# Performance work log

Measured on AMD Instinct MI355X. Metric: run time of the kernel, lower is better.

## Reference

```python
import jax, jax.numpy as jnp
import numpy as np
import itertools

B = 128
K = 3            # number of element types == len(n_list)
C_IN = 256
C_OUT = 256
N_LIST = [3, 3, 3]  # L = 9, P = 9!/(3!3!3!) = 1680


def _build_mask():
    # multiset [0,0,0,1,1,1,2,2,2]; distinct permutations of it
    base = []
    for i, n in enumerate(N_LIST):
        base += [i] * n
    perms = sorted(set(itertools.permutations(base)))  # deterministic order
    idx = np.array(perms, dtype=np.int32)              # (P, L)
    # M[a, p, l] = 1.0 iff idx[p, l] == a  -> (K, P, L) binary mask
    M = np.stack([(idx == a).astype(np.float32) for a in range(K)], 0)
    return jnp.asarray(M), idx.shape[1]


def setup_inputs() -> dict:
    key = jax.random.key(0)
    kx, kw = jax.random.split(key)
    M, L = _build_mask()
    x = jax.random.normal(kx, (B, L, C_IN), dtype=jnp.float32)
    # weightParameter: (k, channels_out, channels_in)
    W = jax.random.normal(kw, (K, C_OUT, C_IN), dtype=jnp.float32)
    return {"x": x, "W": W, "M": M}


def reference(x, W, M):
    # Original: for each type a, W_a = x @ W[a].T (B,L,Cout), then
    # y += einsum('BNC,PN->BPC', W_a, M[a]).  Fused over the k loop:
    # Z[b,l,a,o] = sum_c x[b,l,c] * W[a,o,c]   (small: B*L*K*Cout)
    Z = jnp.einsum('blc,koc->blko', x, W)
    # y[b,p,o] = sum_{a,l} Z[b,l,a,o] * M[a,p,l]
    y = jnp.einsum('blko,kpl->bpo', Z, M)
    return y
```

## Files before the change

kernel.cpp:

```cpp
#include <hip/hip_runtime.h>

#define B_DIM 128
#define L_DIM 9
#define K_DIM 3
#define C 256
#define P_TOT 1680
#define R_DIM 27
#define CHUNK 210

#define WS_WT_OFF 16384
#define WS_Z_OFF  (1u << 20)

typedef float vfloat4 __attribute__((ext_vector_type(4)));

__device__ inline float4 add4(float4 a, float4 b) {
    return make_float4(a.x + b.x, a.y + b.y, a.z + b.z, a.w + b.w);
}

__global__ __launch_bounds__(256) void setup_kernel(const float* __restrict__ M,
                                                    const float* __restrict__ W,
                                                    uint2* __restrict__ packed,
                                                    float* __restrict__ Wt) {
    int bid = blockIdx.x;
    int t = threadIdx.x;
    if (bid < 7) {
        int p = bid * 256 + t;
        if (p >= P_TOT) return;
        unsigned rows[L_DIM];
#pragma unroll
        for (int l = 0; l < L_DIM; ++l) {
            float m1 = M[(1 * P_TOT + p) * L_DIM + l];
            float m2 = M[(2 * P_TOT + p) * L_DIM + l];
            unsigned a = (unsigned)(m1 + 2.0f * m2 + 0.5f);
            rows[l] = (unsigned)(l * K_DIM) + a;
        }
        unsigned d = 0;
        if (p > 0) {
            while (d < L_DIM) {
                float m1 = M[(1 * P_TOT + (p - 1)) * L_DIM + d];
                float m2 = M[(2 * P_TOT + (p - 1)) * L_DIM + d];
                unsigned pr = d * K_DIM + (unsigned)(m1 + 2.0f * m2 + 0.5f);
                if (pr != rows[d]) break;
                ++d;
            }
        }
        unsigned lo = 0, hi = 0;
#pragma unroll
        for (int l = 0; l < 6; ++l) lo |= rows[l] << (5 * l);
#pragma unroll
        for (int l = 6; l < L_DIM; ++l) hi |= rows[l] << (5 * (l - 6));
        hi |= d << 15;
        packed[p] = make_uint2(lo, hi);
    } else {
        int tb = bid - 7;
#pragma unroll
        for (int i = 0; i < 4; ++i) {
            int rowid = tb * 4 + i;
            int a = rowid >> 8;
            int c = rowid & 255;
            Wt[(a * C + c) * C + t] = W[(a * C + t) * C + c];
        }
    }
}

__global__ __launch_bounds__(384) void z_kernel(const float* __restrict__ x,
                                                const float* __restrict__ Wt,
                                                float* __restrict__ Z) {
    int bid = blockIdx.x;
    int b = bid >> 1;
    int t = threadIdx.x;
    int a = t >> 7;
    int o = ((bid & 1) << 7) + (t & 127);

    const float4* __restrict__ xb4 = (const float4*)(x + (size_t)b * (L_DIM * C));
    const float* __restrict__ wp = Wt + (size_t)a * C * C + o;

    float acc[L_DIM];
#pragma unroll
    for (int l = 0; l < L_DIM; ++l) acc[l] = 0.0f;

#pragma unroll 2
    for (int c4 = 0; c4 < C / 4; ++c4) {
        float w0 = wp[(4 * c4 + 0) * C];
        float w1 = wp[(4 * c4 + 1) * C];
        float w2 = wp[(4 * c4 + 2) * C];
        float w3 = wp[(4 * c4 + 3) * C];
#pragma unroll
        for (int l = 0; l < L_DIM; ++l) {
            float4 xv = xb4[l * (C / 4) + c4];
            acc[l] += xv.x * w0 + xv.y * w1 + xv.z * w2 + xv.w * w3;
        }
    }
#pragma unroll
    for (int l = 0; l < L_DIM; ++l)
        Z[((size_t)b * R_DIM + (l * K_DIM + a)) * C + o] = acc[l];
}

__global__ __launch_bounds__(256) void stream_kernel(const float* __restrict__ Z,
                                                     const uint2* __restrict__ packed,
                                                     float* __restrict__ out) {
    __shared__ float Zs[R_DIM * C];
    __shared__ uint2 pk[CHUNK];

    int bid = blockIdx.x;
    int b = bid >> 3;
    int pstart = (bid & 7) * CHUNK;
    int t = threadIdx.x;

    const float4* zg = (const float4*)(Z + (size_t)b * R_DIM * C);
#pragma unroll
    for (int k = 0; k < 7; ++k) {
        int idx = k * 256 + t;
        if (idx < R_DIM * C / 4) ((float4*)Zs)[idx] = zg[idx];
    }
    if (t < CHUNK) pk[t] = packed[pstart + t];
    __syncthreads();

    int wave = t >> 6;
    int lane = t & 63;
    const float4* zsr = (const float4*)Zs;
    vfloat4* out4 = (vfloat4*)out;

    int pb = (CHUNK * wave) >> 2;
    int pe = (CHUNK * (wave + 1)) >> 2;

    float4 p0, p1, p2, p3, p4, p5, p6, p7, p8;

    for (int pl = pb; pl < pe; ++pl) {
        uint2 w = pk[pl];
        unsigned lo = __builtin_amdgcn_readfirstlane(w.x);
        unsigned hi = __builtin_amdgcn_readfirstlane(w.y);
        int k = (pl == pb) ? 0 : (int)(hi >> 15);
        switch (k) {
            case 0: p0 = zsr[(lo & 31u) * 64 + lane]; [[fallthrough]];
            case 1: p1 = add4(p0, zsr[((lo >> 5) & 31u) * 64 + lane]); [[fallthrough]];
            case 2: p2 = add4(p1, zsr[((lo >> 10) & 31u) * 64 + lane]); [[fallthrough]];
            case 3: p3 = add4(p2, zsr[((lo >> 15) & 31u) * 64 + lane]); [[fallthrough]];
            case 4: p4 = add4(p3, zsr[((lo >> 20) & 31u) * 64 + lane]); [[fallthrough]];
            case 5: p5 = add4(p4, zsr[((lo >> 25) & 31u) * 64 + lane]); [[fallthrough]];
            case 6: p6 = add4(p5, zsr[(hi & 31u) * 64 + lane]); [[fallthrough]];
            case 7: p7 = add4(p6, zsr[((hi >> 5) & 31u) * 64 + lane]); [[fallthrough]];
            case 8: p8 = add4(p7, zsr[((hi >> 10) & 31u) * 64 + lane]); break;
            default: break;
        }
        size_t orow = (size_t)(b * P_TOT + pstart + pl);
        vfloat4 sv = {p8.x, p8.y, p8.z, p8.w};
        __builtin_nontemporal_store(sv, &out4[orow * 64 + lane]);
    }
}

extern "C" void kernel_launch(void* const* d_in, const int* in_sizes, int n_in,
                              void* d_out, int out_size, void* d_ws, size_t ws_size,
                              hipStream_t stream) {
    const float* x = (const float*)d_in[0];
    const float* W = (const float*)d_in[1];
    const float* M = (const float*)d_in[2];
    float* out = (float*)d_out;

    uint2* packed = (uint2*)d_ws;
    float* Wt = (float*)((char*)d_ws + WS_WT_OFF);
    float* Z = (float*)((char*)d_ws + WS_Z_OFF);

    setup_kernel<<<199, 256, 0, stream>>>(M, W, packed, Wt);
    z_kernel<<<256, 384, 0, stream>>>(x, Wt, Z);
    stream_kernel<<<1024, 256, 0, stream>>>(Z, packed, out);
}
```

Before: 272.0 us.

## Replace prefix-sum reuse with pairwise-sum lookup table in stream kernel

Instead of reusing prefix sums across consecutive permutations, each block builds a shared-memory table of all pairwise sums for four position pairs (36 rows) plus the last position's three rows. Each output row then takes five table loads and four adds with a single 32-bit packed index, rather than a variable-length chain of up to nine loads with a divergent switch. The stream kernel also moves to 512-thread blocks with 420-row chunks, halving the block count. The cost is the table-building prologue per block and more shared memory. The kernel is output-store bound, so the gain depends on whether the loop was limited by issue or by memory.

```diff
diff --git a/kernel.cpp b/kernel.cpp
--- a/kernel.cpp
+++ b/kernel.cpp
@@ -6,7 +6,8 @@
 #define C 256
 #define P_TOT 1680
 #define R_DIM 27
-#define CHUNK 210
+#define CHUNK 420
+#define LUT_ROWS 39
 
 #define WS_WT_OFF 16384
 #define WS_Z_OFF  (1u << 20)
@@ -19,46 +20,34 @@
 
 __global__ __launch_bounds__(256) void setup_kernel(const float* __restrict__ M,
                                                     const float* __restrict__ W,
-                                                    uint2* __restrict__ packed,
+                                                    unsigned* __restrict__ pkg,
                                                     float* __restrict__ Wt) {
     int bid = blockIdx.x;
     int t = threadIdx.x;
     if (bid < 7) {
         int p = bid * 256 + t;
         if (p >= P_TOT) return;
-        unsigned rows[L_DIM];
+        unsigned a[L_DIM];
 #pragma unroll
         for (int l = 0; l < L_DIM; ++l) {
             float m1 = M[(1 * P_TOT + p) * L_DIM + l];
             float m2 = M[(2 * P_TOT + p) * L_DIM + l];
-            unsigned a = (unsigned)(m1 + 2.0f * m2 + 0.5f);
-            rows[l] = (unsigned)(l * K_DIM) + a;
+            a[l] = (unsigned)(m1 + 2.0f * m2 + 0.5f);
         }
-        unsigned d = 0;
-        if (p > 0) {
-            while (d < L_DIM) {
-                float m1 = M[(1 * P_TOT + (p - 1)) * L_DIM + d];
-                float m2 = M[(2 * P_TOT + (p - 1)) * L_DIM + d];
-                unsigned pr = d * K_DIM + (unsigned)(m1 + 2.0f * m2 + 0.5f);
-                if (pr != rows[d]) break;
-                ++d;
-            }
-        }
-        unsigned lo = 0, hi = 0;
+        unsigned w = 0;
 #pragma unroll
-        for (int l = 0; l < 6; ++l) lo |= rows[l] << (5 * l);
-#pragma unroll
-        for (int l = 6; l < L_DIM; ++l) hi |= rows[l] << (5 * (l - 6));
-        hi |= d << 15;
-        packed[p] = make_uint2(lo, hi);
+        for (int j = 0; j < 4; ++j)
+            w |= (unsigned)(j * 9 + a[2 * j] * 3 + a[2 * j + 1]) << (6 * j);
+        w |= (36u + a[8]) << 24;
+        pkg[p] = w;
     } else {
         int tb = bid - 7;
 #pragma unroll
         for (int i = 0; i < 4; ++i) {
             int rowid = tb * 4 + i;
-            int a = rowid >> 8;
+            int aa = rowid >> 8;
             int c = rowid & 255;
-            Wt[(a * C + c) * C + t] = W[(a * C + t) * C + c];
+            Wt[(aa * C + c) * C + t] = W[(aa * C + t) * C + c];
         }
     }
 }
@@ -96,55 +85,59 @@
         Z[((size_t)b * R_DIM + (l * K_DIM + a)) * C + o] = acc[l];
 }
 
-__global__ __launch_bounds__(256) void stream_kernel(const float* __restrict__ Z,
-                                                     const uint2* __restrict__ packed,
+__global__ __launch_bounds__(512) void stream_kernel(const float* __restrict__ Z,
+                                                     const unsigned* __restrict__ pkg,
                                                      float* __restrict__ out) {
-    __shared__ float Zs[R_DIM * C];
-    __shared__ uint2 pk[CHUNK];
+    __shared__ float lut[LUT_ROWS * C];
+    __shared__ unsigned pk[CHUNK];
 
     int bid = blockIdx.x;
-    int b = bid >> 3;
-    int pstart = (bid & 7) * CHUNK;
+    int b = bid >> 2;
+    int pstart = (bid & 3) * CHUNK;
     int t = threadIdx.x;
 
     const float4* zg = (const float4*)(Z + (size_t)b * R_DIM * C);
+    float4* lutw = (float4*)lut;
 #pragma unroll
-    for (int k = 0; k < 7; ++k) {
-        int idx = k * 256 + t;
-        if (idx < R_DIM * C / 4) ((float4*)Zs)[idx] = zg[idx];
+    for (int it = 0; it < 5; ++it) {
+        int idx = it * 512 + t;
+        if (idx < LUT_ROWS * 64) {
+            int r = idx >> 6, q = idx & 63;
+            float4 v;
+            if (r < 36) {
+                int j = r / 9;
+                int cmb = r - j * 9;
+                int a0 = cmb / 3;
+                int a1 = cmb - a0 * 3;
+                v = add4(zg[(6 * j + a0) * 64 + q], zg[(6 * j + 3 + a1) * 64 + q]);
+            } else {
+                v = zg[(24 + r - 36) * 64 + q];
+            }
+            lutw[idx] = v;
+        }
     }
-    if (t < CHUNK) pk[t] = packed[pstart + t];
+    if (t < CHUNK) pk[t] = pkg[pstart + t];
     __syncthreads();
 
     int wave = t >> 6;
     int lane = t & 63;
-    const float4* zsr = (const float4*)Zs;
+    const float4* lutr = (const float4*)lut;
     vfloat4* out4 = (vfloat4*)out;
 
-    int pb = (CHUNK * wave) >> 2;
-    int pe = (CHUNK * (wave + 1)) >> 2;
+    int pb = (CHUNK * wave) >> 3;
+    int pe = (CHUNK * (wave + 1)) >> 3;
 
-    float4 p0, p1, p2, p3, p4, p5, p6, p7, p8;
-
+#pragma unroll 2
     for (int pl = pb; pl < pe; ++pl) {
-        uint2 w = pk[pl];
-        unsigned lo = __builtin_amdgcn_readfirstlane(w.x);
-        unsigned hi = __builtin_amdgcn_readfirstlane(w.y);
-        int k = (pl == pb) ? 0 : (int)(hi >> 15);
-        switch (k) {
-            case 0: p0 = zsr[(lo & 31u) * 64 + lane]; [[fallthrough]];
-            case 1: p1 = add4(p0, zsr[((lo >> 5) & 31u) * 64 + lane]); [[fallthrough]];
-            case 2: p2 = add4(p1, zsr[((lo >> 10) & 31u) * 64 + lane]); [[fallthrough]];
-            case 3: p3 = add4(p2, zsr[((lo >> 15) & 31u) * 64 + lane]); [[fallthrough]];
-            case 4: p4 = add4(p3, zsr[((lo >> 20) & 31u) * 64 + lane]); [[fallthrough]];
-            case 5: p5 = add4(p4, zsr[((lo >> 25) & 31u) * 64 + lane]); [[fallthrough]];
-            case 6: p6 = add4(p5, zsr[(hi & 31u) * 64 + lane]); [[fallthrough]];
-            case 7: p7 = add4(p6, zsr[((hi >> 5) & 31u) * 64 + lane]); [[fallthrough]];
-            case 8: p8 = add4(p7, zsr[((hi >> 10) & 31u) * 64 + lane]); break;
-            default: break;
-        }
+        unsigned w = __builtin_amdgcn_readfirstlane(pk[pl]);
+        float4 v0 = lutr[((w)&63u) * 64 + lane];
+        float4 v1 = lutr[((w >> 6) & 63u) * 64 + lane];
+        float4 v2 = lutr[((w >> 12) & 63u) * 64 + lane];
+        float4 v3 = lutr[((w >> 18) & 63u) * 64 + lane];
+        float4 v4 = lutr[((w >> 24) & 63u) * 64 + lane];
+        float4 s = add4(add4(add4(v0, v1), add4(v2, v3)), v4);
         size_t orow = (size_t)(b * P_TOT + pstart + pl);
-        vfloat4 sv = {p8.x, p8.y, p8.z, p8.w};
+        vfloat4 sv = {s.x, s.y, s.z, s.w};
         __builtin_nontemporal_store(sv, &out4[orow * 64 + lane]);
     }
 }
@@ -157,11 +150,11 @@
     const float* M = (const float*)d_in[2];
     float* out = (float*)d_out;
 
-    uint2* packed = (uint2*)d_ws;
+    unsigned* pkg = (unsigned*)d_ws;
     float* Wt = (float*)((char*)d_ws + WS_WT_OFF);
     float* Z = (float*)((char*)d_ws + WS_Z_OFF);
 
-    setup_kernel<<<199, 256, 0, stream>>>(M, W, packed, Wt);
+    setup_kernel<<<199, 256, 0, stream>>>(M, W, pkg, Wt);
     z_kernel<<<256, 384, 0, stream>>>(x, Wt, Z);
-    stream_kernel<<<1024, 256, 0, stream>>>(Z, packed, out);
+    stream_kernel<<<512, 512, 0, stream>>>(Z, pkg, out);
 }
```

Result: faster. 262.8 us (-3.4%).
